# Optimization experiments

Measured on AMD Instinct MI355X. Metric: run time of the kernel, lower is better.

The kernel has to match this reference:

```python
import jax, jax.numpy as jnp
import numpy as np

N, E, D, M, R, NH, HD, FF = 20000, 160000, 64, 4, 5, 4, 16, 16


def _ln(x, g, b, eps=1e-5):
    mu = x.mean(-1, keepdims=True)
    var = ((x - mu) ** 2).mean(-1, keepdims=True)
    return (x - mu) / jnp.sqrt(var + eps) * g + b


def _encoder(x, p):
    # Post-norm nn.TransformerEncoderLayer(D, nhead=4, dim_feedforward=16), eval mode.
    # x: (B, 4, D); returns CLS output (B, D). Padding mask is all-zeros -> no masking.
    B = x.shape[0]
    qkv = x @ p['in_w'].T + p['in_b']                     # (B,4,3D)
    q, k, v = jnp.split(qkv, 3, axis=-1)
    hview = lambda t: t.reshape(B, 4, NH, HD).transpose(0, 2, 1, 3)  # (B,H,4,hd)
    q, k, v = hview(q), hview(k), hview(v)
    attn = jax.nn.softmax(jnp.einsum('bhqd,bhkd->bhqk', q, k) / jnp.sqrt(jnp.float32(HD)), axis=-1)
    o = jnp.einsum('bhqk,bhkd->bhqd', attn, v).transpose(0, 2, 1, 3).reshape(B, 4, D)
    o = o @ p['out_w'].T + p['out_b']
    x = _ln(x + o, p['ln1_g'], p['ln1_b'])
    ff = jax.nn.relu(x @ p['ff1_w'].T + p['ff1_b']) @ p['ff2_w'].T + p['ff2_b']
    x = _ln(x + ff, p['ln2_g'], p['ln2_b'])
    return x[:, 0, :]


def _mem_encode(h_a, h_b, cls_w, sep, p):
    # For each memory slot m: encode [CLS_m, h_a, SEP, h_b]; sum CLS outputs.
    B = h_a.shape[0]
    sep_t = jnp.broadcast_to(sep, (B, 1, D))
    outs = []
    mem_emb = jnp.zeros((B, D), h_a.dtype)
    for m in range(M):  # small fixed loop over memory slots
        cls_t = jnp.broadcast_to(cls_w[m], (B, 1, D))
        seq = jnp.concatenate([cls_t, h_a[:, None, :], sep_t, h_b[:, None, :]], axis=1)
        t = _encoder(seq, p)
        outs.append(t)
        mem_emb = mem_emb + t
    return mem_emb, outs


def setup_inputs() -> dict:
    key = jax.random.key(0)
    ks = jax.random.split(key, 16)
    s = 0.05
    f32 = jnp.float32
    inp = {}
    inp['feat'] = jax.random.normal(ks[0], (N, D), f32)
    inp['src'] = jax.random.randint(ks[1], (E,), 0, N, dtype=jnp.int32)
    inp['dst'] = jax.random.randint(ks[2], (E,), 0, N, dtype=jnp.int32)
    inp['etype'] = jax.random.randint(ks[3], (E,), 0, R, dtype=jnp.int32)
    inp['cls_w'] = jax.random.normal(ks[4], (M, D), f32)           # CLS embedding, std=1 as in source
    inp['sep'] = jax.random.normal(ks[5], (D,), f32)
    inp['in_w'] = jax.random.normal(ks[6], (3 * D, D), f32) * s
    inp['in_b'] = jnp.zeros((3 * D,), f32)
    inp['out_w'] = jax.random.normal(ks[7], (D, D), f32) * s
    inp['out_b'] = jnp.zeros((D,), f32)
    inp['ln1_g'] = jnp.ones((D,), f32)
    inp['ln1_b'] = jnp.zeros((D,), f32)
    inp['ln2_g'] = jnp.ones((D,), f32)
    inp['ln2_b'] = jnp.zeros((D,), f32)
    inp['ff1_w'] = jax.random.normal(ks[8], (FF, D), f32) * s
    inp['ff1_b'] = jnp.zeros((FF,), f32)
    inp['ff2_w'] = jax.random.normal(ks[9], (D, FF), f32) * s
    inp['ff2_b'] = jnp.zeros((D,), f32)
    inp['memcat_w'] = jax.random.normal(ks[10], (M, D), f32) * s
    inp['memcat_b'] = jnp.zeros((M,), f32)
    inp['memw_w'] = jax.random.normal(ks[11], (D * D, D), f32) * s
    inp['h_bias'] = jnp.zeros((D,), f32)
    inp['lnw_g'] = jnp.ones((D,), f32)
    inp['lnw_b'] = jnp.zeros((D,), f32)
    return inp


def reference(feat, src, dst, etype, cls_w, sep, in_w, in_b, out_w, out_b,
              ln1_g, ln1_b, ln2_g, ln2_b, ff1_w, ff1_b, ff2_w, ff2_b,
              memcat_w, memcat_b, memw_w, h_bias, lnw_g, lnw_b):
    p = dict(in_w=in_w, in_b=in_b, out_w=out_w, out_b=out_b, ln1_g=ln1_g, ln1_b=ln1_b,
             ln2_g=ln2_g, ln2_b=ln2_b, ff1_w=ff1_w, ff1_b=ff1_b, ff2_w=ff2_w, ff2_b=ff2_b)
    h_src = feat[src]                                      # (E,D) gather
    h_dst = feat[dst]
    # Per-etype loop in the source uses identical params for every edge, so the message
    # math vectorizes over all edges; only category/label ordering depends on etype.
    mem_emb, outs = _mem_encode(h_src, h_dst, cls_w, sep, p)   # (E,D)
    cat_all = jnp.stack([t @ memcat_w.T + memcat_b for t in outs])  # (M,E,mem_size)
    # Reproduce source ordering: for etype e (ascending), for slot m, edges in original order.
    counts = jnp.bincount(etype, length=R)
    start = jnp.cumsum(counts) - counts                    # exclusive prefix
    perm = jnp.argsort(etype)                              # stable sort by etype
    e_s = etype[perm]
    local = jnp.arange(E) - start[e_s]
    pos = M * start[e_s][None, :] + jnp.arange(M)[:, None] * counts[e_s][None, :] + local[None, :]  # (M,E)
    category = jnp.zeros((M * E, M), cat_all.dtype).at[pos.reshape(-1)].set(cat_all[:, perm].reshape(M * E, M))
    label = jnp.zeros((M * E,), jnp.int32).at[pos.reshape(-1)].set(
        jnp.broadcast_to(jnp.arange(M, dtype=jnp.int32)[:, None], (M, E)).reshape(-1))
    # Dynamic per-edge weight + message
    w = (mem_emb @ memw_w.T).reshape(-1, D, D)             # (E, out, in)
    msg = jnp.einsum('eoi,ei->eo', w, h_src)               # (E,D)
    # fn.mean aggregation (zero-degree nodes -> 0, matching DGL)
    deg = jax.ops.segment_sum(jnp.ones((E,), feat.dtype), dst, num_segments=N)
    agg = jax.ops.segment_sum(msg, dst, num_segments=N) / jnp.maximum(deg, 1.0)[:, None]
    node = _ln(agg, lnw_g, lnw_b) + h_bias
    # self-loop branch: same memory-slot transformer on (feat, feat)
    mem_emb_n, _ = _mem_encode(feat, feat, cls_w, sep, p)
    w_n = (mem_emb_n @ memw_w.T).reshape(-1, D, D)
    node = node + jnp.einsum('noi,ni->no', w_n, feat)
    node = jnp.where(node > 0, node, 0.2 * node)           # LeakyReLU(0.2); dropout is identity in eval
    return node, category, label
```

## Files before the change

kernel.cpp:

```cpp
#include <hip/hip_runtime.h>

#define DI __device__ __forceinline__

static constexpr int NN = 20000;
static constexpr int NE = 160000;

typedef __attribute__((ext_vector_type(4))) float f32x4;
typedef _Float16 f16x2 __attribute__((ext_vector_type(2)));
typedef _Float16 f16x8 __attribute__((ext_vector_type(8)));

DI float rl(float v, int lane) {
    return __int_as_float(__builtin_amdgcn_readlane(__float_as_int(v), lane));
}
DI float xr(float v, int m) { return __shfl_xor(v, m, 64); }
DI float wsum64(float v) {
    v += xr(v, 1); v += xr(v, 2); v += xr(v, 4);
    v += xr(v, 8); v += xr(v, 16); v += xr(v, 32);
    return v;
}
DI float hsum16(float v) {
    v += xr(v, 1); v += xr(v, 2); v += xr(v, 4); v += xr(v, 8);
    return v;
}
DI float hsum16d(float v) {
    v += __int_as_float(__builtin_amdgcn_mov_dpp(__float_as_int(v), 0xB1, 0xF, 0xF, true));
    v += __int_as_float(__builtin_amdgcn_mov_dpp(__float_as_int(v), 0x4E, 0xF, 0xF, true));
    v += __int_as_float(__builtin_amdgcn_mov_dpp(__float_as_int(v), 0x141, 0xF, 0xF, true));
    v += __int_as_float(__builtin_amdgcn_mov_dpp(__float_as_int(v), 0x140, 0xF, 0xF, true));
    return v;
}
DI float wsum64v(float v) {
    v = hsum16d(v);
    return (rl(v, 0) + rl(v, 16)) + (rl(v, 32) + rl(v, 48));
}
DI unsigned short f2h(float x) {
    union { _Float16 f; unsigned short u; } c;
    c.f = (_Float16)x;
    return c.u;
}

__global__ __launch_bounds__(256) void prepA_kernel(
    const float* __restrict__ mw, unsigned short* __restrict__ Wstg,
    const float* __restrict__ in_w, const float* __restrict__ out_w,
    float* __restrict__ WOVg,
    const float* __restrict__ cls_w, const float* __restrict__ sep,
    const float* __restrict__ in_b, float* __restrict__ P,
    const int* __restrict__ et, int* __restrict__ bc,
    const int* __restrict__ dstp, float* __restrict__ deg) {
    int b = blockIdx.x, t = threadIdx.x;
    __shared__ int c[5];
    if (b < 1024) {
        int idx = b * 256 + t;
        int d = idx & 63, o = (idx >> 6) & 63, i = idx >> 12;
        Wstg[idx] = f2h(mw[(o * 64 + i) * 64 + d]);
    } else if (b < 1088) {
        int u = (b - 1024) * 256 + t;
        int h = u & 3, l = (u >> 2) & 63, j = u >> 8;
        float acc = 0.f;
        for (int i = 0; i < 16; i++)
            acc += out_w[l * 64 + h * 16 + i] * in_w[(128 + h * 16 + i) * 64 + j];
        WOVg[u] = acc;
    } else if (b == 1088) {
        if (t < 64) {
            int l = t;
            float bq = in_b[l], bk = in_b[64 + l], bv = in_b[128 + l];
            float xs = sep[l];
            float ks = bk, vs = bv;
            for (int j = 0; j < 64; j++) {
                float xj = rl(xs, j);
                ks += in_w[(64 + l) * 64 + j] * xj;
                vs += in_w[(128 + l) * 64 + j] * xj;
            }
            P[512 + l] = vs;
            for (int m = 0; m < 4; m++) {
                float xc = cls_w[m * 64 + l];
                float q0 = bq, kc = bk, vc = bv;
                for (int j = 0; j < 64; j++) {
                    float xj = rl(xc, j);
                    q0 += in_w[l * 64 + j] * xj;
                    kc += in_w[(64 + l) * 64 + j] * xj;
                    vc += in_w[(128 + l) * 64 + j] * xj;
                }
                P[m * 64 + l] = q0;
                P[256 + m * 64 + l] = vc;
                float p0 = hsum16(q0 * kc);
                float p2 = hsum16(q0 * ks);
                if ((l & 15) == 0) {
                    P[576 + m * 4 + (l >> 4)] = p0 * 0.25f;
                    P[592 + m * 4 + (l >> 4)] = p2 * 0.25f;
                }
            }
        }
    } else if (b < 1714) {
        int bb = b - 1089;
        if (t < 5) c[t] = 0;
        __syncthreads();
        int e = bb * 256 + t;
        if (e < NE) atomicAdd(&c[et[e]], 1);
        __syncthreads();
        if (t < 5) bc[bb * 5 + t] = c[t];
    } else {
        int e = (b - 1714) * 256 + t;
        if (e < NE) atomicAdd(&deg[dstp[e]], 1.0f);
    }
}

__global__ __launch_bounds__(256) void prepB_kernel(
    const float* __restrict__ in_w, const float* __restrict__ in_b,
    const float* __restrict__ out_w,
    const float* __restrict__ mc_w, const float* __restrict__ mc_b,
    const float* __restrict__ ln1_g, const float* __restrict__ ln1_b,
    const float* __restrict__ ln2_g, const float* __restrict__ ln2_b,
    const float* __restrict__ ff1_w, const float* __restrict__ ff1_b,
    const float* __restrict__ cls_w, const float* __restrict__ out_b,
    const float* __restrict__ P,
    float* __restrict__ SWg, float* __restrict__ SB16,
    float* __restrict__ OvcG, float* __restrict__ OvsG,
    float* __restrict__ bOvG, float* __restrict__ s0n,
    float* __restrict__ s2n, float* __restrict__ MC8,
    float* __restrict__ GcT, float* __restrict__ GsT,
    float* __restrict__ DCC, float* __restrict__ B0T,
    float* __restrict__ mgT,
    const int* __restrict__ bc, int* __restrict__ boff, int* __restrict__ cs, int nb) {
    int t = threadIdx.x;
    if (blockIdx.x == 1) {
        if (t < 5) {
            int tot = 0;
            for (int b = 0; b < nb; b++) { boff[b * 5 + t] = tot; tot += bc[b * 5 + t]; }
            cs[t] = tot;
        }
        __syncthreads();
        if (t == 0) {
            int s = 0;
            for (int e = 0; e < 5; e++) { cs[5 + e] = s; s += cs[e]; }
        }
        return;
    }
    for (int u = t; u < 1024; u += 256) {
        int m = u >> 8, h = (u >> 6) & 3, j = u & 63;
        float acc = 0.f;
        for (int i = 0; i < 16; i++)
            acc += P[m * 64 + h * 16 + i] * in_w[(64 + h * 16 + i) * 64 + j];
        SWg[u] = 0.25f * acc;
    }
    for (int u = t; u < 1024; u += 256) {
        int h = u & 3, ll = (u >> 2) & 63, m = u >> 8;
        float acc = 0.f;
        for (int i = 0; i < 16; i++)
            acc += out_w[ll * 64 + h * 16 + i] * P[256 + m * 64 + h * 16 + i];
        OvcG[u] = acc;
    }
    if (t < 256) {
        int h = t & 3, ll = t >> 2;
        float a1 = 0.f, a2 = 0.f;
        for (int i = 0; i < 16; i++) {
            a1 += out_w[ll * 64 + h * 16 + i] * P[512 + h * 16 + i];
            a2 += out_w[ll * 64 + h * 16 + i] * in_b[128 + h * 16 + i];
        }
        OvsG[t] = a1;
        bOvG[t] = a2;
    }
    if (t < 256) {
        B0T[t] = cls_w[t] + out_b[t & 63];
        int p = t >> 2, cc = t & 3;
        mgT[t] = mc_w[cc * 64 + p] * ln2_g[p];
    }
    if (t < 16) {
        int m = t >> 2, h = t & 3;
        float acc = 0.f;
        for (int i = 0; i < 16; i++)
            acc += P[m * 64 + h * 16 + i] * in_b[64 + h * 16 + i];
        SB16[t] = 0.25f * acc;
        s0n[t] = P[576 + t];
        s2n[t] = P[592 + t];
    }
    if (t < 8) {
        int cc = t & 3;
        float acc = 0.f;
        if (t < 4) {
            for (int ll = 0; ll < 64; ll++) acc += mc_w[cc * 64 + ll] * ln2_g[ll];
        } else {
            for (int ll = 0; ll < 64; ll++) acc += mc_w[cc * 64 + ll] * ln2_b[ll];
            acc += mc_b[cc];
        }
        MC8[t] = acc;
    }
    __syncthreads();
    if (t < 256) {
        int m = t >> 6, f = (t >> 2) & 15, h = t & 3;
        float acc = 0.f;
        for (int p = 0; p < 64; p++)
            acc += ff1_w[f * 64 + p] * ln1_g[p] * OvcG[(m * 64 + p) * 4 + h];
        GcT[t] = acc;
    }
    if (t < 64) {
        int f = t >> 2, h = t & 3;
        float acc = 0.f;
        for (int p = 0; p < 64; p++)
            acc += ff1_w[f * 64 + p] * ln1_g[p] * OvsG[p * 4 + h];
        GsT[t] = acc;
    }
    if (t < 64) {
        int m = t >> 4, f = t & 15;
        float d0 = 0.f, c1 = 0.f, c2 = 0.f;
        for (int p = 0; p < 64; p++) {
            float wv = ff1_w[f * 64 + p];
            d0 += wv * ln1_g[p] * (cls_w[m * 64 + p] + out_b[p]);
            c1 += wv * ln1_g[p];
            c2 += wv * ln1_b[p];
        }
        f32x4 r = {d0, c1, c2 + ff1_b[f], 0.f};
        ((f32x4*)DCC)[t] = r;
    }
}

__global__ __launch_bounds__(256) void prepC_kernel(
    const int* __restrict__ et, const int* __restrict__ boff,
    const int* __restrict__ cs, int* __restrict__ rowbase,
    int* __restrict__ estride,
    const float* __restrict__ feat, const float* __restrict__ SWg,
    const float* __restrict__ SB16, const float* __restrict__ WOVg,
    const float* __restrict__ bOvG, const float* __restrict__ ff1_w,
    const float* __restrict__ ln1_g,
    float* __restrict__ Sout, float* __restrict__ Ovout, float* __restrict__ Gn) {
    __shared__ float SWs[1024];
    __shared__ f32x4 WOVs[4096];
    __shared__ __align__(16) float F1gL[1024];
    __shared__ __align__(16) float accT[4][4][64];
    __shared__ int wc[4][5];
    int tid = threadIdx.x;
    if (blockIdx.x < 625) {
        int b = blockIdx.x;
        int w = tid >> 6, lane = tid & 63;
        int e = b * 256 + tid;
        bool valid = e < NE;
        int my = valid ? et[e] : 0;
        unsigned long long bal[5];
#pragma unroll
        for (int ty = 0; ty < 5; ty++) bal[ty] = __ballot(valid && my == ty);
        if (lane == 0) {
#pragma unroll
            for (int ty = 0; ty < 5; ty++) wc[w][ty] = __popcll(bal[ty]);
        }
        __syncthreads();
        if (valid) {
            unsigned long long lt = ((unsigned long long)1 << lane) - 1;
            int intra = __popcll(bal[my] & lt);
            int pre = 0;
            for (int w2 = 0; w2 < w; w2++) pre += wc[w2][my];
            rowbase[e] = 4 * cs[5 + my] + boff[b * 5 + my] + pre + intra;
            estride[e] = cs[my];
        }
        return;
    }
    int nb4 = blockIdx.x - 625;
    for (int p = tid; p < 1024; p += 256) {
        SWs[p] = SWg[p];
        F1gL[p] = ff1_w[p] * ln1_g[p & 63];
    }
    for (int p = tid; p < 4096; p += 256) WOVs[p] = ((const f32x4*)WOVg)[p];
    __syncthreads();
    int w = tid >> 6, l = tid & 63;
    int n = nb4 * 4 + w;
    float f = feat[(size_t)n * 64 + l];
    f32x4 acc = ((const f32x4*)bOvG)[l];
#pragma unroll 8
    for (int j = 0; j < 64; j++) {
        float fj = rl(f, j);
        f32x4 wv = WOVs[j * 64 + l];
        acc += wv * fj;
    }
    ((f32x4*)Ovout)[(size_t)n * 64 + l] = acc;
    accT[w][0][l] = acc[0];
    accT[w][1][l] = acc[1];
    accT[w][2][l] = acc[2];
    accT[w][3][l] = acc[3];
#pragma unroll
    for (int mh = 0; mh < 16; mh++) {
        float v = SWs[mh * 64 + l] * f;
        v = wsum64v(v);
        if (l == mh) Sout[(size_t)n * 16 + mh] = v + SB16[mh];
    }
    asm volatile("s_waitcnt lgkmcnt(0)" ::: "memory");
    int ff = l & 15, hh = l >> 4;
    float g = 0.f;
#pragma unroll
    for (int c = 0; c < 16; c++) {
        int cc = (c + ff) & 15;
        f32x4 wv = *(const f32x4*)&F1gL[ff * 64 + cc * 4];
        f32x4 av = *(const f32x4*)&accT[w][hh][cc * 4];
        g += wv[0] * av[0] + wv[1] * av[1] + wv[2] * av[2] + wv[3] * av[3];
    }
    Gn[(size_t)n * 64 + ff * 4 + hh] = g;
}

__global__ __launch_bounds__(256, 4) void enc_kernel(
    const int* __restrict__ src, const int* __restrict__ dst,
    const float* __restrict__ Sg, const float* __restrict__ Ovg,
    const float* __restrict__ Gn, const float* __restrict__ OvcG,
    const float* __restrict__ OvsG, const float* __restrict__ GcT,
    const float* __restrict__ GsT, const float* __restrict__ DCC,
    const float* __restrict__ B0T, const float* __restrict__ mgT,
    const float* __restrict__ s0n, const float* __restrict__ s2n,
    const float* __restrict__ MC8,
    const float* __restrict__ ln1_g, const float* __restrict__ ln1_b,
    const float* __restrict__ ln2_g, const float* __restrict__ ln2_b,
    const float* __restrict__ ff2_w, const float* __restrict__ ff2_b,
    const int* __restrict__ rowbase, const int* __restrict__ estride,
    float* __restrict__ mem_out, float* __restrict__ out_cat,
    float* __restrict__ out_label) {
    __shared__ __align__(16) float F2C[1024];
    __shared__ __align__(16) float TBL[1704];
    int tid = threadIdx.x;
    for (int p = tid; p < 1024; p += 256) F2C[(p & 15) * 64 + (p >> 4)] = ff2_w[p];
    {
        f32x4* T4w = (f32x4*)TBL;
        int i = tid;
        if (i < 64) {
            T4w[i]        = ((const f32x4*)B0T)[i];
            T4w[64 + i]   = ((const f32x4*)GcT)[i];
            T4w[128 + i]  = ((const f32x4*)DCC)[i];
            T4w[192 + (i & 3) * 16 + (i >> 2)] = ((const f32x4*)OvsG)[i];
            T4w[256 + (i & 3) * 16 + (i >> 2)] = ((const f32x4*)mgT)[i];
        }
        if (i < 16) {
            T4w[320 + i] = ((const f32x4*)GsT)[i];
            T4w[346 + i] = *(const f32x4*)(ln1_g + i * 4);
            T4w[362 + i] = *(const f32x4*)(ln1_b + i * 4);
            T4w[378 + i] = *(const f32x4*)(ln2_g + i * 4);
            T4w[394 + i] = *(const f32x4*)(ln2_b + i * 4);
            T4w[410 + i] = *(const f32x4*)(ff2_b + i * 4);
        }
        if (i < 4) {
            T4w[336 + i] = ((const f32x4*)s0n)[i];
            T4w[340 + i] = ((const f32x4*)s2n)[i];
        }
        if (i < 2) T4w[344 + i] = ((const f32x4*)MC8)[i];
    }
    __syncthreads();
    const f32x4* F2C4 = (const f32x4*)F2C;
    const f32x4* Sg4 = (const f32x4*)Sg;
    const f32x4* Og4 = (const f32x4*)Ovg;
    const f32x4* Gn4 = (const f32x4*)Gn;

    int l = tid & 63, m = l >> 4, u = l & 15;
    f32x4 OvcR0 = ((const f32x4*)OvcG)[m * 64 + u * 4 + 0];
    f32x4 OvcR1 = ((const f32x4*)OvcG)[m * 64 + u * 4 + 1];
    f32x4 OvcR2 = ((const f32x4*)OvcG)[m * 64 + u * 4 + 2];
    f32x4 OvcR3 = ((const f32x4*)OvcG)[m * 64 + u * 4 + 3];
    int ubase = u * 17;
    int wid = blockIdx.x * 4 + (tid >> 6);
    int nw = gridDim.x * 4;

    for (int it = wid; it < NE + NN; it += nw) {
        int tb = 0;
        asm volatile("" : "+v"(tb));
        const f32x4* T4 = ((const f32x4*)TBL) + tb;
        int itu = __builtin_amdgcn_readfirstlane(it);
        bool isE = itu < NE;
        int ia = isE ? src[itu] : (itu - NE);
        f32x4 SaV = Sg4[(size_t)ia * 4 + m];
        f32x4 GaV = Gn4[(size_t)ia * 16 + u];
        f32x4 OvaR0 = Og4[(size_t)ia * 64 + u * 4 + 0];
        f32x4 OvaR1 = Og4[(size_t)ia * 64 + u * 4 + 1];
        f32x4 OvaR2 = Og4[(size_t)ia * 64 + u * 4 + 2];
        f32x4 OvaR3 = Og4[(size_t)ia * 64 + u * 4 + 3];
        f32x4 SbV = SaV, GbV = GaV;
        f32x4 OvbR0 = OvaR0, OvbR1 = OvaR1, OvbR2 = OvaR2, OvbR3 = OvaR3;
        int rb = 0, st = 0;
        if (isE) {
            int ib = dst[itu];
            SbV = Sg4[(size_t)ib * 4 + m];
            GbV = Gn4[(size_t)ib * 16 + u];
            OvbR0 = Og4[(size_t)ib * 64 + u * 4 + 0];
            OvbR1 = Og4[(size_t)ib * 64 + u * 4 + 1];
            OvbR2 = Og4[(size_t)ib * 64 + u * 4 + 2];
            OvbR3 = Og4[(size_t)ib * 64 + u * 4 + 3];
            rb = rowbase[itu];
            st = estride[itu];
        }
        f32x4 s0v = T4[336 + m];
        f32x4 s2v = T4[340 + m];
        f32x4 B0v = T4[l];
        f32x4 GcV = T4[64 + l];
        f32x4 DCv = T4[128 + l];
        f32x4 GsV = T4[320 + u];
        f32x4 OvsR0 = T4[192 + u];
        f32x4 OvsR1 = T4[208 + u];
        f32x4 OvsR2 = T4[224 + u];
        f32x4 OvsR3 = T4[240 + u];

        f32x4 mx, e0, e1, e2, e3, w0v, w1v, w2v, w3v;
#pragma unroll
        for (int h = 0; h < 4; h++)
            mx[h] = fmaxf(fmaxf(s0v[h], SaV[h]), fmaxf(s2v[h], SbV[h]));
#pragma unroll
        for (int h = 0; h < 4; h++) {
            e0[h] = __expf(s0v[h] - mx[h]);
            e1[h] = __expf(SaV[h] - mx[h]);
            e2[h] = __expf(s2v[h] - mx[h]);
            e3[h] = __expf(SbV[h] - mx[h]);
        }
#pragma unroll
        for (int h = 0; h < 4; h++) {
            float inv = 1.f / (e0[h] + e1[h] + e2[h] + e3[h]);
            w0v[h] = e0[h] * inv; w1v[h] = e1[h] * inv;
            w2v[h] = e2[h] * inv; w3v[h] = e3[h] * inv;
        }
        f32x4 xv = B0v;
#pragma unroll
        for (int h = 0; h < 4; h++) {
            float W0 = w0v[h], W1 = w1v[h], W2 = w2v[h], W3 = w3v[h];
            xv[0] += W0 * OvcR0[h] + W1 * OvaR0[h] + W2 * OvsR0[h] + W3 * OvbR0[h];
            xv[1] += W0 * OvcR1[h] + W1 * OvaR1[h] + W2 * OvsR1[h] + W3 * OvbR1[h];
            xv[2] += W0 * OvcR2[h] + W1 * OvaR2[h] + W2 * OvsR2[h] + W3 * OvbR2[h];
            xv[3] += W0 * OvcR3[h] + W1 * OvaR3[h] + W2 * OvsR3[h] + W3 * OvbR3[h];
        }
        float sx = hsum16d(xv[0] + xv[1] + xv[2] + xv[3]);
        float sxx = hsum16d(xv[0] * xv[0] + xv[1] * xv[1] + xv[2] * xv[2] + xv[3] * xv[3]);
        float mu = sx * 0.015625f;
        float var = sxx * 0.015625f - mu * mu;
        float r1 = rsqrtf(var + 1e-5f);
        f32x4 av = w0v * GcV + w1v * GaV + w2v * GsV + w3v * GbV;
        float accF = av[0] + av[1] + av[2] + av[3] + DCv[0];
        float hp = r1 * accF - (r1 * mu) * DCv[1] + DCv[2];
        float hr = fmaxf(hp, 0.f);
        f32x4 g1r = T4[346 + u], b1r = T4[362 + u], f2br = T4[410 + u];
        xv = (xv - mu) * (g1r * r1) + b1r;
        f32x4 yv = xv + f2br;
        float hrot = hr;
        int a16 = ubase + tb;
        { f32x4 wv = F2C4[a16]; yv += wv * hrot; }
#define FSTEP(CTL, MSK)                                                                         \
        hrot = __int_as_float(__builtin_amdgcn_mov_dpp(__float_as_int(hrot), (CTL), 0xF, 0xF, true)); \
        a16 ^= (MSK) * 16;                                                                      \
        { f32x4 wv = F2C4[a16]; yv += wv * hrot; }
        FSTEP(0xB1, 1) FSTEP(0x4E, 2) FSTEP(0xB1, 1) FSTEP(0x141, 7)
        FSTEP(0xB1, 1) FSTEP(0x4E, 2) FSTEP(0xB1, 1) FSTEP(0x140, 15)
        FSTEP(0xB1, 1) FSTEP(0x4E, 2) FSTEP(0xB1, 1) FSTEP(0x141, 7)
        FSTEP(0xB1, 1) FSTEP(0x4E, 2) FSTEP(0xB1, 1)
#undef FSTEP
        float sy = hsum16d(yv[0] + yv[1] + yv[2] + yv[3]);
        float syy = hsum16d(yv[0] * yv[0] + yv[1] * yv[1] + yv[2] * yv[2] + yv[3] * yv[3]);
        float mu2 = sy * 0.015625f;
        float var2 = syy * 0.015625f - mu2 * mu2;
        float r2 = rsqrtf(var2 + 1e-5f);
        f32x4 g2r = T4[378 + u], b2r = T4[394 + u];
        f32x4 tv = (yv - mu2) * (g2r * r2) + b2r;
        f32x4 mem4;
#pragma unroll
        for (int k = 0; k < 4; k++) {
            float s = tv[k];
            s += xr(s, 16);
            s += xr(s, 32);
            mem4[k] = s;
        }
        if (m == 0) *(f32x4*)(mem_out + (size_t)itu * 64 + u * 4) = mem4;
        if (isE) {
            f32x4 mg0 = T4[256 + u];
            f32x4 mg1 = T4[272 + u];
            f32x4 mg2 = T4[288 + u];
            f32x4 mg3 = T4[304 + u];
            f32x4 pcv = yv[0] * mg0 + yv[1] * mg1 + yv[2] * mg2 + yv[3] * mg3;
            f32x4 McV = T4[344];
            f32x4 CcV = T4[345];
            f32x4 dv;
            dv[0] = hsum16d(pcv[0]);
            dv[1] = hsum16d(pcv[1]);
            dv[2] = hsum16d(pcv[2]);
            dv[3] = hsum16d(pcv[3]);
            f32x4 cv = (dv - McV * mu2) * r2 + CcV;
            int row = rb + m * st;
            if (u == 0) {
                *(f32x4*)(out_cat + (size_t)row * 4) = cv;
                out_label[row] = (float)m;
            }
        }
    }
}

__global__ __launch_bounds__(256, 2) void msg_kernel(
    const float* __restrict__ feat, const int* __restrict__ src, const int* __restrict__ dstv,
    const float* __restrict__ mem_all, const unsigned short* __restrict__ Wstg,
    float* __restrict__ agg, float* __restrict__ msg_n) {
    constexpr int RS = 72;
    constexpr int EB = NE / 256;
    __shared__ __align__(16) unsigned short Wt[4 * 64 * RS];
    __shared__ unsigned hTu[4 * 256];
    int tid = threadIdx.x;
    int w = tid >> 6, lane = tid & 63;
    int m16 = lane & 15, q = lane >> 4;
    bool isE = blockIdx.x < EB;
    int blockbase = (isE ? blockIdx.x : blockIdx.x - EB) * 256;
    int count = isE ? NE : NN;
    size_t moff = isE ? 0 : (size_t)NE;
    int wavebase = w * 64;

    f16x2 mpk[4][2][4];
#pragma unroll
    for (int Mt = 0; Mt < 4; Mt++) {
        int it = blockbase + wavebase + Mt * 16 + m16;
        if (it >= count) it = count - 1;
        const float* mrow = mem_all + (moff + (size_t)it) * 64;
#pragma unroll
        for (int ks = 0; ks < 2; ks++) {
            float4 a = *(const float4*)(mrow + ks * 32 + q * 8);
            float4 b = *(const float4*)(mrow + ks * 32 + q * 8 + 4);
            mpk[Mt][ks][0] = f16x2{(_Float16)a.x, (_Float16)a.y};
            mpk[Mt][ks][1] = f16x2{(_Float16)a.z, (_Float16)a.w};
            mpk[Mt][ks][2] = f16x2{(_Float16)b.x, (_Float16)b.y};
            mpk[Mt][ks][3] = f16x2{(_Float16)b.z, (_Float16)b.w};
        }
    }
    f32x4 acc[4][4];
#pragma unroll
    for (int Mt = 0; Mt < 4; Mt++)
#pragma unroll
        for (int nt = 0; nt < 4; nt++) {
            f32x4 z = {0.f, 0.f, 0.f, 0.f};
            acc[Mt][nt] = z;
        }

    for (int ch = 0; ch < 16; ch++) {
        __syncthreads();
        const unsigned short* gsl = Wstg + (size_t)ch * 4 * 4096;
#pragma unroll
        for (int p = 0; p < 8; p++) {
            int flat = p * 2048 + tid * 8;
            int ic = flat >> 12, o = (flat >> 6) & 63, d = flat & 63;
            uint4 v = *(const uint4*)(gsl + flat);
            *(uint4*)&Wt[(ic * 64 + o) * RS + d] = v;
        }
        {
            int it = blockbase + tid;
            if (it >= count) it = count - 1;
            int hidx = isE ? src[it] : it;
            float4 hv = *(const float4*)(feat + (size_t)hidx * 64 + ch * 4);
            union { f16x2 f; unsigned u; } d0, d1, d2, d3;
            d0.f = f16x2{(_Float16)hv.x, (_Float16)hv.x};
            d1.f = f16x2{(_Float16)hv.y, (_Float16)hv.y};
            d2.f = f16x2{(_Float16)hv.z, (_Float16)hv.z};
            d3.f = f16x2{(_Float16)hv.w, (_Float16)hv.w};
            hTu[0 * 256 + tid] = d0.u;
            hTu[1 * 256 + tid] = d1.u;
            hTu[2 * 256 + tid] = d2.u;
            hTu[3 * 256 + tid] = d3.u;
        }
        __syncthreads();

#pragma unroll
        for (int il = 0; il < 4; il++) {
            f16x8 afr[4][2];
#pragma unroll
            for (int Mt = 0; Mt < 4; Mt++) {
                union { f16x2 f; unsigned u; } hh;
                hh.u = hTu[il * 256 + wavebase + Mt * 16 + m16];
                f16x2 hd = hh.f;
#pragma unroll
                for (int ks = 0; ks < 2; ks++) {
                    union { unsigned u[4]; f16x8 v; } uu;
#pragma unroll
                    for (int jj = 0; jj < 4; jj++) {
                        union { f16x2 f; unsigned u; } rr;
                        rr.f = mpk[Mt][ks][jj] * hd;
                        uu.u[jj] = rr.u;
                    }
                    afr[Mt][ks] = uu.v;
                }
            }
            const unsigned short* wrow = &Wt[(il * 64) * RS];
#pragma unroll
            for (int nt = 0; nt < 4; nt++) {
#pragma unroll
                for (int ks = 0; ks < 2; ks++) {
                    int o = nt * 16 + m16;
                    union { uint4 u; f16x8 v; } bb;
                    bb.u = *(const uint4*)&wrow[o * RS + ks * 32 + q * 8];
#pragma unroll
                    for (int Mt = 0; Mt < 4; Mt++)
                        acc[Mt][nt] = __builtin_amdgcn_mfma_f32_16x16x32_f16(
                            afr[Mt][ks], bb.v, acc[Mt][nt], 0, 0, 0);
                }
            }
        }
    }
#pragma unroll
    for (int Mt = 0; Mt < 4; Mt++) {
        int ib = blockbase + wavebase + Mt * 16 + q * 4;
        if (!isE) {
#pragma unroll
            for (int r = 0; r < 4; r++) {
                int it = ib + r;
                if (it < count) {
#pragma unroll
                    for (int nt = 0; nt < 4; nt++)
                        msg_n[(size_t)it * 64 + nt * 16 + m16] = acc[Mt][nt][r];
                }
            }
        } else {
            int4 dd = *(const int4*)(dstv + ib);
#pragma unroll
            for (int r = 0; r < 4; r++) {
                int dn = (&dd.x)[r];
#pragma unroll
                for (int nt = 0; nt < 4; nt++)
                    atomicAdd(&agg[(size_t)dn * 64 + nt * 16 + m16], acc[Mt][nt][r]);
            }
        }
    }
}

__global__ __launch_bounds__(256) void final_kernel(
    const float* __restrict__ agg, const float* __restrict__ deg, const float* __restrict__ msgn,
    const float* __restrict__ lnw_g, const float* __restrict__ lnw_b,
    const float* __restrict__ h_bias, float* __restrict__ outp, int nN) {
    int tid = threadIdx.x, w = tid >> 6, l = tid & 63;
    int n = blockIdx.x * 4 + w;
    if (n >= nN) return;
    float a = agg[(size_t)n * 64 + l] / fmaxf(deg[n], 1.f);
    float mu = wsum64(a) * (1.f / 64.f);
    float d = a - mu;
    float var = wsum64(d * d) * (1.f / 64.f);
    float v = d * rsqrtf(var + 1e-5f) * lnw_g[l] + lnw_b[l] + h_bias[l] + msgn[(size_t)n * 64 + l];
    outp[(size_t)n * 64 + l] = v > 0.f ? v : 0.2f * v;
}


extern "C" void kernel_launch(void* const* d_in, const int* in_sizes, int n_in,
                              void* d_out, int out_size, void* d_ws, size_t ws_size,
                              hipStream_t stream) {
    const float* feat   = (const float*)d_in[0];
    const int*   src    = (const int*)d_in[1];
    const int*   dst    = (const int*)d_in[2];
    const int*   etype  = (const int*)d_in[3];
    const float* cls_w  = (const float*)d_in[4];
    const float* sep    = (const float*)d_in[5];
    const float* in_w   = (const float*)d_in[6];
    const float* in_b   = (const float*)d_in[7];
    const float* out_w  = (const float*)d_in[8];
    const float* out_b  = (const float*)d_in[9];
    const float* ln1_g  = (const float*)d_in[10];
    const float* ln1_b  = (const float*)d_in[11];
    const float* ln2_g  = (const float*)d_in[12];
    const float* ln2_b  = (const float*)d_in[13];
    const float* ff1_w  = (const float*)d_in[14];
    const float* ff1_b  = (const float*)d_in[15];
    const float* ff2_w  = (const float*)d_in[16];
    const float* ff2_b  = (const float*)d_in[17];
    const float* mc_w   = (const float*)d_in[18];
    const float* mc_b   = (const float*)d_in[19];
    const float* memw_w = (const float*)d_in[20];
    const float* h_bias = (const float*)d_in[21];
    const float* lnw_g  = (const float*)d_in[22];
    const float* lnw_b  = (const float*)d_in[23];

    char* ws = (char*)d_ws;
    size_t off = 0;
    auto nxt = [&](size_t bytes) -> void* {
        void* p = ws + off;
        off += (bytes + 255) & ~(size_t)255;
        return p;
    };
    unsigned short* Wstg = (unsigned short*)nxt(64 * 64 * 64 * sizeof(unsigned short));
    float* P       = (float*)nxt(1024 * sizeof(float));
    float* SWg     = (float*)nxt(1024 * sizeof(float));
    float* SB16    = (float*)nxt(16 * sizeof(float));
    float* OvcG    = (float*)nxt(1024 * sizeof(float));
    float* OvsG    = (float*)nxt(256 * sizeof(float));
    float* bOvG    = (float*)nxt(256 * sizeof(float));
    float* s0n     = (float*)nxt(16 * sizeof(float));
    float* s2n     = (float*)nxt(16 * sizeof(float));
    float* MC8     = (float*)nxt(8 * sizeof(float));
    float* GcT     = (float*)nxt(256 * sizeof(float));
    float* GsT     = (float*)nxt(64 * sizeof(float));
    float* DCC     = (float*)nxt(256 * sizeof(float));
    float* B0T     = (float*)nxt(256 * sizeof(float));
    float* mgT     = (float*)nxt(256 * sizeof(float));
    float* WOVg    = (float*)nxt(16384 * sizeof(float));
    float* Sg      = (float*)nxt((size_t)NN * 16 * sizeof(float));
    float* Ovg     = (float*)nxt((size_t)NN * 256 * sizeof(float));
    float* Gn      = (float*)nxt((size_t)NN * 64 * sizeof(float));
    int*   bc      = (int*)nxt(625 * 5 * sizeof(int));
    int*   boff    = (int*)nxt(625 * 5 * sizeof(int));
    int*   cs      = (int*)nxt(16 * sizeof(int));
    int*   rowbase = (int*)nxt((size_t)NE * sizeof(int));
    int*   estride = (int*)nxt((size_t)NE * sizeof(int));
    float* mem_all = (float*)nxt((size_t)(NE + NN) * 64 * sizeof(float));
    float* agg     = (float*)nxt((size_t)NN * 64 * sizeof(float));
    float* deg     = (float*)nxt((size_t)NN * sizeof(float));
    float* msg_n   = (float*)nxt((size_t)NN * 64 * sizeof(float));
    (void)ws_size; (void)in_sizes; (void)n_in; (void)out_size;

    float* out_node  = (float*)d_out;
    float* out_cat   = out_node + (size_t)NN * 64;
    float* out_label = out_cat + (size_t)4 * NE * 4;

    hipMemsetAsync(agg, 0, (size_t)NN * 64 * sizeof(float), stream);
    hipMemsetAsync(deg, 0, (size_t)NN * sizeof(float), stream);

    prepA_kernel<<<2339, 256, 0, stream>>>(memw_w, Wstg, in_w, out_w, WOVg,
                                           cls_w, sep, in_b, P, etype, bc, dst, deg);
    prepB_kernel<<<2, 256, 0, stream>>>(in_w, in_b, out_w, mc_w, mc_b,
                                        ln1_g, ln1_b, ln2_g, ln2_b, ff1_w, ff1_b,
                                        cls_w, out_b, P,
                                        SWg, SB16, OvcG, OvsG, bOvG, s0n, s2n, MC8,
                                        GcT, GsT, DCC, B0T, mgT,
                                        bc, boff, cs, 625);
    prepC_kernel<<<5625, 256, 0, stream>>>(etype, boff, cs, rowbase, estride,
                                           feat, SWg, SB16, WOVg, bOvG, ff1_w, ln1_g,
                                           Sg, Ovg, Gn);
    enc_kernel<<<2048, 256, 0, stream>>>(
        src, dst, Sg, Ovg, Gn, OvcG, OvsG, GcT, GsT, DCC, B0T, mgT, s0n, s2n, MC8,
        ln1_g, ln1_b, ln2_g, ln2_b, ff2_w, ff2_b,
        rowbase, estride, mem_all, out_cat, out_label);
    msg_kernel<<<625 + (NN + 255) / 256, 256, 0, stream>>>(
        feat, src, dst, mem_all, Wstg, agg, msg_n);

    final_kernel<<<(NN + 3) / 4, 256, 0, stream>>>(agg, deg, msg_n, lnw_g, lnw_b, h_bias, out_node, NN);
}
```

Baseline: 548.2 us.

## Merge prep kernels and memsets into fewer launches, compute offsets per block

```diff
diff --git a/kernel.cpp b/kernel.cpp
--- a/kernel.cpp
+++ b/kernel.cpp
@@ -13,9 +13,15 @@
     return __int_as_float(__builtin_amdgcn_readlane(__float_as_int(v), lane));
 }
 DI float xr(float v, int m) { return __shfl_xor(v, m, 64); }
+DI int xri(int v, int m) { return __shfl_xor(v, m, 64); }
 DI float wsum64(float v) {
     v += xr(v, 1); v += xr(v, 2); v += xr(v, 4);
     v += xr(v, 8); v += xr(v, 16); v += xr(v, 32);
+    return v;
+}
+DI int wsum64i(int v) {
+    v += xri(v, 1); v += xri(v, 2); v += xri(v, 4);
+    v += xri(v, 8); v += xri(v, 16); v += xri(v, 32);
     return v;
 }
 DI float hsum16(float v) {
@@ -44,11 +50,24 @@
     const float* __restrict__ in_w, const float* __restrict__ out_w,
     float* __restrict__ WOVg,
     const float* __restrict__ cls_w, const float* __restrict__ sep,
-    const float* __restrict__ in_b, float* __restrict__ P,
+    const float* __restrict__ in_b,
     const int* __restrict__ et, int* __restrict__ bc,
-    const int* __restrict__ dstp, float* __restrict__ deg) {
+    float* __restrict__ agg, float* __restrict__ deg,
+    const float* __restrict__ mc_w, const float* __restrict__ mc_b,
+    const float* __restrict__ ln1_g, const float* __restrict__ ln1_b,
+    const float* __restrict__ ln2_g, const float* __restrict__ ln2_b,
+    const float* __restrict__ ff1_w, const float* __restrict__ ff1_b,
+    const float* __restrict__ out_b,
+    float* __restrict__ SWg, float* __restrict__ SB16,
+    float* __restrict__ OvcG, float* __restrict__ OvsG,
+    float* __restrict__ bOvG, float* __restrict__ s0n,
+    float* __restrict__ s2n, float* __restrict__ MC8,
+    float* __restrict__ GcT, float* __restrict__ GsT,
+    float* __restrict__ DCC, float* __restrict__ B0T,
+    float* __restrict__ mgT) {
     int b = blockIdx.x, t = threadIdx.x;
     __shared__ int c[5];
+    __shared__ float P[608];
     if (b < 1024) {
         int idx = b * 256 + t;
         int d = idx & 63, o = (idx >> 6) & 63, i = idx >> 12;
@@ -91,133 +110,108 @@
                 }
             }
         }
+        __syncthreads();
+        for (int u = t; u < 1024; u += 256) {
+            int m = u >> 8, h = (u >> 6) & 3, j = u & 63;
+            float acc = 0.f;
+            for (int i = 0; i < 16; i++)
+                acc += P[m * 64 + h * 16 + i] * in_w[(64 + h * 16 + i) * 64 + j];
+            SWg[u] = 0.25f * acc;
+        }
+        for (int u = t; u < 1024; u += 256) {
+            int h = u & 3, ll = (u >> 2) & 63, m = u >> 8;
+            float acc = 0.f;
+            for (int i = 0; i < 16; i++)
+                acc += out_w[ll * 64 + h * 16 + i] * P[256 + m * 64 + h * 16 + i];
+            OvcG[u] = acc;
+        }
+        if (t < 256) {
+            int h = t & 3, ll = t >> 2;
+            float a1 = 0.f, a2 = 0.f;
+            for (int i = 0; i < 16; i++) {
+                a1 += out_w[ll * 64 + h * 16 + i] * P[512 + h * 16 + i];
+                a2 += out_w[ll * 64 + h * 16 + i] * in_b[128 + h * 16 + i];
+            }
+            OvsG[t] = a1;
+            bOvG[t] = a2;
+        }
+        if (t < 256) {
+            B0T[t] = cls_w[t] + out_b[t & 63];
+            int p = t >> 2, cc = t & 3;
+            mgT[t] = mc_w[cc * 64 + p] * ln2_g[p];
+        }
+        if (t < 16) {
+            int m = t >> 2, h = t & 3;
+            float acc = 0.f;
+            for (int i = 0; i < 16; i++)
+                acc += P[m * 64 + h * 16 + i] * in_b[64 + h * 16 + i];
+            SB16[t] = 0.25f * acc;
+            s0n[t] = P[576 + t];
+            s2n[t] = P[592 + t];
+        }
+        if (t < 8) {
+            int cc = t & 3;
+            float acc = 0.f;
+            if (t < 4) {
+                for (int ll = 0; ll < 64; ll++) acc += mc_w[cc * 64 + ll] * ln2_g[ll];
+            } else {
+                for (int ll = 0; ll < 64; ll++) acc += mc_w[cc * 64 + ll] * ln2_b[ll];
+                acc += mc_b[cc];
+            }
+            MC8[t] = acc;
+        }
+        __syncthreads();
+        if (t < 256) {
+            int m = t >> 6, f = (t >> 2) & 15, h = t & 3;
+            float acc = 0.f;
+            for (int p = 0; p < 64; p++)
+                acc += ff1_w[f * 64 + p] * ln1_g[p] * OvcG[(m * 64 + p) * 4 + h];
+            GcT[t] = acc;
+        }
+        if (t < 64) {
+            int f = t >> 2, h = t & 3;
+            float acc = 0.f;
+            for (int p = 0; p < 64; p++)
+                acc += ff1_w[f * 64 + p] * ln1_g[p] * OvsG[p * 4 + h];
+            GsT[t] = acc;
+        }
+        if (t < 64) {
+            int m = t >> 4, f = t & 15;
+            float d0 = 0.f, c1 = 0.f, c2 = 0.f;
+            for (int p = 0; p < 64; p++) {
+                float wv = ff1_w[f * 64 + p];
+                d0 += wv * ln1_g[p] * (cls_w[m * 64 + p] + out_b[p]);
+                c1 += wv * ln1_g[p];
+                c2 += wv * ln1_b[p];
+            }
+            f32x4 r = {d0, c1, c2 + ff1_b[f], 0.f};
+            ((f32x4*)DCC)[t] = r;
+        }
     } else if (b < 1714) {
         int bb = b - 1089;
         if (t < 5) c[t] = 0;
         __syncthreads();
         int e = bb * 256 + t;
-        if (e < NE) atomicAdd(&c[et[e]], 1);
+        atomicAdd(&c[et[e]], 1);
         __syncthreads();
         if (t < 5) bc[bb * 5 + t] = c[t];
+    } else if (b < 2964) {
+        int idx = (b - 1714) * 256 + t;
+        f32x4 z = {0.f, 0.f, 0.f, 0.f};
+        ((f32x4*)agg)[idx] = z;
     } else {
-        int e = (b - 1714) * 256 + t;
-        if (e < NE) atomicAdd(&deg[dstp[e]], 1.0f);
-    }
-}
-
-__global__ __launch_bounds__(256) void prepB_kernel(
-    const float* __restrict__ in_w, const float* __restrict__ in_b,
-    const float* __restrict__ out_w,
-    const float* __restrict__ mc_w, const float* __restrict__ mc_b,
-    const float* __restrict__ ln1_g, const float* __restrict__ ln1_b,
-    const float* __restrict__ ln2_g, const float* __restrict__ ln2_b,
-    const float* __restrict__ ff1_w, const float* __restrict__ ff1_b,
-    const float* __restrict__ cls_w, const float* __restrict__ out_b,
-    const float* __restrict__ P,
-    float* __restrict__ SWg, float* __restrict__ SB16,
-    float* __restrict__ OvcG, float* __restrict__ OvsG,
-    float* __restrict__ bOvG, float* __restrict__ s0n,
-    float* __restrict__ s2n, float* __restrict__ MC8,
-    float* __restrict__ GcT, float* __restrict__ GsT,
-    float* __restrict__ DCC, float* __restrict__ B0T,
-    float* __restrict__ mgT,
-    const int* __restrict__ bc, int* __restrict__ boff, int* __restrict__ cs, int nb) {
-    int t = threadIdx.x;
-    if (blockIdx.x == 1) {
-        if (t < 5) {
-            int tot = 0;
-            for (int b = 0; b < nb; b++) { boff[b * 5 + t] = tot; tot += bc[b * 5 + t]; }
-            cs[t] = tot;
-        }
-        __syncthreads();
-        if (t == 0) {
-            int s = 0;
-            for (int e = 0; e < 5; e++) { cs[5 + e] = s; s += cs[e]; }
-        }
-        return;
-    }
-    for (int u = t; u < 1024; u += 256) {
-        int m = u >> 8, h = (u >> 6) & 3, j = u & 63;
-        float acc = 0.f;
-        for (int i = 0; i < 16; i++)
-            acc += P[m * 64 + h * 16 + i] * in_w[(64 + h * 16 + i) * 64 + j];
-        SWg[u] = 0.25f * acc;
-    }
-    for (int u = t; u < 1024; u += 256) {
-        int h = u & 3, ll = (u >> 2) & 63, m = u >> 8;
-        float acc = 0.f;
-        for (int i = 0; i < 16; i++)
-            acc += out_w[ll * 64 + h * 16 + i] * P[256 + m * 64 + h * 16 + i];
-        OvcG[u] = acc;
-    }
-    if (t < 256) {
-        int h = t & 3, ll = t >> 2;
-        float a1 = 0.f, a2 = 0.f;
-        for (int i = 0; i < 16; i++) {
-            a1 += out_w[ll * 64 + h * 16 + i] * P[512 + h * 16 + i];
-            a2 += out_w[ll * 64 + h * 16 + i] * in_b[128 + h * 16 + i];
-        }
-        OvsG[t] = a1;
-        bOvG[t] = a2;
-    }
-    if (t < 256) {
-        B0T[t] = cls_w[t] + out_b[t & 63];
-        int p = t >> 2, cc = t & 3;
-        mgT[t] = mc_w[cc * 64 + p] * ln2_g[p];
-    }
-    if (t < 16) {
-        int m = t >> 2, h = t & 3;
-        float acc = 0.f;
-        for (int i = 0; i < 16; i++)
-            acc += P[m * 64 + h * 16 + i] * in_b[64 + h * 16 + i];
-        SB16[t] = 0.25f * acc;
-        s0n[t] = P[576 + t];
-        s2n[t] = P[592 + t];
-    }
-    if (t < 8) {
-        int cc = t & 3;
-        float acc = 0.f;
-        if (t < 4) {
-            for (int ll = 0; ll < 64; ll++) acc += mc_w[cc * 64 + ll] * ln2_g[ll];
-        } else {
-            for (int ll = 0; ll < 64; ll++) acc += mc_w[cc * 64 + ll] * ln2_b[ll];
-            acc += mc_b[cc];
-        }
-        MC8[t] = acc;
-    }
-    __syncthreads();
-    if (t < 256) {
-        int m = t >> 6, f = (t >> 2) & 15, h = t & 3;
-        float acc = 0.f;
-        for (int p = 0; p < 64; p++)
-            acc += ff1_w[f * 64 + p] * ln1_g[p] * OvcG[(m * 64 + p) * 4 + h];
-        GcT[t] = acc;
-    }
-    if (t < 64) {
-        int f = t >> 2, h = t & 3;
-        float acc = 0.f;
-        for (int p = 0; p < 64; p++)
-            acc += ff1_w[f * 64 + p] * ln1_g[p] * OvsG[p * 4 + h];
-        GsT[t] = acc;
-    }
-    if (t < 64) {
-        int m = t >> 4, f = t & 15;
-        float d0 = 0.f, c1 = 0.f, c2 = 0.f;
-        for (int p = 0; p < 64; p++) {
-            float wv = ff1_w[f * 64 + p];
-            d0 += wv * ln1_g[p] * (cls_w[m * 64 + p] + out_b[p]);
-            c1 += wv * ln1_g[p];
-            c2 += wv * ln1_b[p];
-        }
-        f32x4 r = {d0, c1, c2 + ff1_b[f], 0.f};
-        ((f32x4*)DCC)[t] = r;
+        int idx = (b - 2964) * 256 + t;
+        if (idx < 5000) {
+            f32x4 z = {0.f, 0.f, 0.f, 0.f};
+            ((f32x4*)deg)[idx] = z;
+        }
     }
 }
 
 __global__ __launch_bounds__(256) void prepC_kernel(
-    const int* __restrict__ et, const int* __restrict__ boff,
-    const int* __restrict__ cs, int* __restrict__ rowbase,
-    int* __restrict__ estride,
+    const int* __restrict__ et, const int* __restrict__ bc,
+    const int* __restrict__ dstp, float* __restrict__ deg,
+    int* __restrict__ rowbase, int* __restrict__ estride,
     const float* __restrict__ feat, const float* __restrict__ SWg,
     const float* __restrict__ SB16, const float* __restrict__ WOVg,
     const float* __restrict__ bOvG, const float* __restrict__ ff1_w,
@@ -228,29 +222,50 @@
     __shared__ __align__(16) float F1gL[1024];
     __shared__ __align__(16) float accT[4][4][64];
     __shared__ int wc[4][5];
+    __shared__ int pre_s[5], tot_s[5], cs5[5];
     int tid = threadIdx.x;
     if (blockIdx.x < 625) {
         int b = blockIdx.x;
+        if (tid < 5) { pre_s[tid] = 0; tot_s[tid] = 0; }
+        __syncthreads();
+#pragma unroll
+        for (int ty = 0; ty < 5; ty++) {
+            int pp = 0, tt = 0;
+            for (int b2 = tid; b2 < 625; b2 += 256) {
+                int v = bc[b2 * 5 + ty];
+                tt += v;
+                if (b2 < b) pp += v;
+            }
+            pp = wsum64i(pp);
+            tt = wsum64i(tt);
+            if ((tid & 63) == 0) {
+                atomicAdd(&pre_s[ty], pp);
+                atomicAdd(&tot_s[ty], tt);
+            }
+        }
+        __syncthreads();
+        if (tid == 0) {
+            int s = 0;
+            for (int e = 0; e < 5; e++) { cs5[e] = s; s += tot_s[e]; }
+        }
         int w = tid >> 6, lane = tid & 63;
         int e = b * 256 + tid;
-        bool valid = e < NE;
-        int my = valid ? et[e] : 0;
+        int my = et[e];
         unsigned long long bal[5];
 #pragma unroll
-        for (int ty = 0; ty < 5; ty++) bal[ty] = __ballot(valid && my == ty);
+        for (int ty = 0; ty < 5; ty++) bal[ty] = __ballot(my == ty);
         if (lane == 0) {
 #pragma unroll
             for (int ty = 0; ty < 5; ty++) wc[w][ty] = __popcll(bal[ty]);
         }
         __syncthreads();
-        if (valid) {
-            unsigned long long lt = ((unsigned long long)1 << lane) - 1;
-            int intra = __popcll(bal[my] & lt);
-            int pre = 0;
-            for (int w2 = 0; w2 < w; w2++) pre += wc[w2][my];
-            rowbase[e] = 4 * cs[5 + my] + boff[b * 5 + my] + pre + intra;
-            estride[e] = cs[my];
-        }
+        unsigned long long lt = ((unsigned long long)1 << lane) - 1;
+        int intra = __popcll(bal[my] & lt);
+        int pre = 0;
+        for (int w2 = 0; w2 < w; w2++) pre += wc[w2][my];
+        rowbase[e] = 4 * cs5[my] + pre_s[my] + pre + intra;
+        estride[e] = tot_s[my];
+        atomicAdd(&deg[dstp[e]], 1.0f);
         return;
     }
     int nb4 = blockIdx.x - 625;
@@ -285,8 +300,8 @@
     int ff = l & 15, hh = l >> 4;
     float g = 0.f;
 #pragma unroll
-    for (int c = 0; c < 16; c++) {
-        int cc = (c + ff) & 15;
+    for (int c2 = 0; c2 < 16; c2++) {
+        int cc = (c2 + ff) & 15;
         f32x4 wv = *(const f32x4*)&F1gL[ff * 64 + cc * 4];
         f32x4 av = *(const f32x4*)&accT[w][hh][cc * 4];
         g += wv[0] * av[0] + wv[1] * av[1] + wv[2] * av[2] + wv[3] * av[3];
@@ -352,6 +367,7 @@
     int wid = blockIdx.x * 4 + (tid >> 6);
     int nw = gridDim.x * 4;
 
+#pragma unroll 2
     for (int it = wid; it < NE + NN; it += nw) {
         int tb = 0;
         asm volatile("" : "+v"(tb));
@@ -500,7 +516,7 @@
 #pragma unroll
     for (int Mt = 0; Mt < 4; Mt++) {
         int it = blockbase + wavebase + Mt * 16 + m16;
-        if (it >= count) it = count - 1;
+        if (!isE && it >= count) it = count - 1;
         const float* mrow = mem_all + (moff + (size_t)it) * 64;
 #pragma unroll
         for (int ks = 0; ks < 2; ks++) {
@@ -533,7 +549,7 @@
         }
         {
             int it = blockbase + tid;
-            if (it >= count) it = count - 1;
+            if (!isE && it >= count) it = count - 1;
             int hidx = isE ? src[it] : it;
             float4 hv = *(const float4*)(feat + (size_t)hidx * 64 + ch * 4);
             union { f16x2 f; unsigned u; } d0, d1, d2, d3;
@@ -662,7 +678,6 @@
         return p;
     };
     unsigned short* Wstg = (unsigned short*)nxt(64 * 64 * 64 * sizeof(unsigned short));
-    float* P       = (float*)nxt(1024 * sizeof(float));
     float* SWg     = (float*)nxt(1024 * sizeof(float));
     float* SB16    = (float*)nxt(16 * sizeof(float));
     float* OvcG    = (float*)nxt(1024 * sizeof(float));
@@ -681,8 +696,6 @@
     float* Ovg     = (float*)nxt((size_t)NN * 256 * sizeof(float));
     float* Gn      = (float*)nxt((size_t)NN * 64 * sizeof(float));
     int*   bc      = (int*)nxt(625 * 5 * sizeof(int));
-    int*   boff    = (int*)nxt(625 * 5 * sizeof(int));
-    int*   cs      = (int*)nxt(16 * sizeof(int));
     int*   rowbase = (int*)nxt((size_t)NE * sizeof(int));
     int*   estride = (int*)nxt((size_t)NE * sizeof(int));
     float* mem_all = (float*)nxt((size_t)(NE + NN) * 64 * sizeof(float));
@@ -695,18 +708,11 @@
     float* out_cat   = out_node + (size_t)NN * 64;
     float* out_label = out_cat + (size_t)4 * NE * 4;
 
-    hipMemsetAsync(agg, 0, (size_t)NN * 64 * sizeof(float), stream);
-    hipMemsetAsync(deg, 0, (size_t)NN * sizeof(float), stream);
-
-    prepA_kernel<<<2339, 256, 0, stream>>>(memw_w, Wstg, in_w, out_w, WOVg,
-                                           cls_w, sep, in_b, P, etype, bc, dst, deg);
-    prepB_kernel<<<2, 256, 0, stream>>>(in_w, in_b, out_w, mc_w, mc_b,
-                                        ln1_g, ln1_b, ln2_g, ln2_b, ff1_w, ff1_b,
-                                        cls_w, out_b, P,
-                                        SWg, SB16, OvcG, OvsG, bOvG, s0n, s2n, MC8,
-                                        GcT, GsT, DCC, B0T, mgT,
-                                        bc, boff, cs, 625);
-    prepC_kernel<<<5625, 256, 0, stream>>>(etype, boff, cs, rowbase, estride,
+    prepA_kernel<<<2984, 256, 0, stream>>>(
+        memw_w, Wstg, in_w, out_w, WOVg, cls_w, sep, in_b, etype, bc, agg, deg,
+        mc_w, mc_b, ln1_g, ln1_b, ln2_g, ln2_b, ff1_w, ff1_b, out_b,
+        SWg, SB16, OvcG, OvsG, bOvG, s0n, s2n, MC8, GcT, GsT, DCC, B0T, mgT);
+    prepC_kernel<<<5625, 256, 0, stream>>>(etype, bc, dst, deg, rowbase, estride,
                                            feat, SWg, SB16, WOVg, bOvG, ff1_w, ln1_g,
                                            Sg, Ovg, Gn);
     enc_kernel<<<2048, 256, 0, stream>>>(
```

Result: faster. 505.6 us, median of 3 (-7.8%).
